# Kernel optimization log

Measured on AMD Instinct MI355X. Metric: run time of the kernel, lower is better.

Reference implementation:

```python
import jax, jax.numpy as jnp
import numpy as np

N_EMBD = 1024
N_HEAD = 16
HEAD_DIM = N_EMBD // N_HEAD


def setup_inputs() -> dict:
    key = jax.random.key(0)
    ks = jax.random.split(key, 9)
    B, T, C = 4, 2048, N_EMBD
    s = 1.0 / np.sqrt(C)
    return {
        "x": jax.random.normal(ks[0], (B, T, C), dtype=jnp.float32),
        "Wk": jax.random.normal(ks[1], (C, C), dtype=jnp.float32) * s,
        "bk": jax.random.normal(ks[2], (C,), dtype=jnp.float32) * 0.02,
        "Wq": jax.random.normal(ks[3], (C, C), dtype=jnp.float32) * s,
        "bq": jax.random.normal(ks[4], (C,), dtype=jnp.float32) * 0.02,
        "Wv": jax.random.normal(ks[5], (C, C), dtype=jnp.float32) * s,
        "bv": jax.random.normal(ks[6], (C,), dtype=jnp.float32) * 0.02,
        "Wp": jax.random.normal(ks[7], (C, C), dtype=jnp.float32) * s,
        "bp": jax.random.normal(ks[8], (C,), dtype=jnp.float32) * 0.02,
    }


def reference(x, Wk, bk, Wq, bq, Wv, bv, Wp, bp):
    B, T, C = x.shape
    nh, hs = N_HEAD, HEAD_DIM
    # linear projections; weights stored as [in, out] (x @ W + b)
    k = (x @ Wk + bk).reshape(B, T, nh, hs).transpose(0, 2, 1, 3)  # [B,nh,T,hs]
    q = (x @ Wq + bq).reshape(B, T, nh, hs).transpose(0, 2, 1, 3)
    v = (x @ Wv + bv).reshape(B, T, nh, hs).transpose(0, 2, 1, 3)
    att = jnp.einsum("bhqd,bhkd->bhqk", q, k) / jnp.sqrt(jnp.float32(hs))
    causal = jnp.tril(jnp.ones((T, T), dtype=bool))  # [T,T]
    att = jnp.where(causal[None, None], att, -jnp.inf)
    att = jax.nn.softmax(att, axis=-1)
    y = jnp.einsum("bhqk,bhkd->bhqd", att, v)  # [B,nh,T,hs]
    y = y.transpose(0, 2, 1, 3).reshape(B, T, C)
    return y @ Wp + bp
```

## Files before the change

### kernel.cpp

```cpp
#include <hip/hip_runtime.h>

#define TSEQ 2048
#define CDIM 1024
#define NH 16
#define HS 64
#define BATCH 4

typedef __attribute__((ext_vector_type(8))) short short8;
typedef __attribute__((ext_vector_type(4))) short s16x4;
typedef __attribute__((ext_vector_type(4))) float f32x4;

__device__ __forceinline__ short f2bf(float f) {
    unsigned u = __builtin_bit_cast(unsigned, f);
    unsigned r = (u + 0x7fffu + ((u >> 16) & 1u)) >> 16;
    return (short)r;
}

__device__ __forceinline__ void gload_lds16(const void* g, void* l) {
    __builtin_amdgcn_global_load_lds((const __attribute__((address_space(1))) void*)g,
                                     (__attribute__((address_space(3))) void*)l, 16, 0, 0);
}

__global__ void cvt_x(const float* __restrict__ x, short* __restrict__ o, int n4) {
    int i = blockIdx.x * 256 + threadIdx.x;
    if (i >= n4) return;
    float4 v = ((const float4*)x)[i];
    s16x4 r;
    r[0] = f2bf(v.x); r[1] = f2bf(v.y); r[2] = f2bf(v.z); r[3] = f2bf(v.w);
    ((s16x4*)o)[i] = r;
}

__global__ void wtrans(const float* __restrict__ Wk, const float* __restrict__ Wq,
                       const float* __restrict__ Wv, const float* __restrict__ Wp,
                       short* __restrict__ Wcat, short* __restrict__ Wpt) {
    const float* src; short* dst;
    if (blockIdx.z == 0)      { src = Wq; dst = Wcat; }
    else if (blockIdx.z == 1) { src = Wk; dst = Wcat + 1048576; }
    else if (blockIdx.z == 2) { src = Wv; dst = Wcat + 2097152; }
    else                      { src = Wp; dst = Wpt; }
    __shared__ float tl[64][65];
    int tx = threadIdx.x & 63, ty = threadIdx.x >> 6;
    int k0 = blockIdx.x * 64, n0 = blockIdx.y * 64;
#pragma unroll
    for (int i = 0; i < 16; ++i) {
        int r = i * 4 + ty;
        tl[r][tx] = src[(size_t)(k0 + r) * CDIM + n0 + tx];
    }
    __syncthreads();
#pragma unroll
    for (int i = 0; i < 16; ++i) {
        int r = i * 4 + ty;
        dst[(size_t)(n0 + r) * CDIM + k0 + tx] = f2bf(tl[tx][r]);
    }
}

__global__ void bias_pack(const float* __restrict__ bq, const float* __restrict__ bk,
                          const float* __restrict__ bv, float* __restrict__ bcat) {
    int i = blockIdx.x * 256 + threadIdx.x;
    if (i < 1024) bcat[i] = bq[i];
    else if (i < 2048) bcat[i] = bk[i - 1024];
    else if (i < 3072) bcat[i] = bv[i - 2048];
}

template <bool OUT_BF16>
__global__ __launch_bounds__(256) void gemm_bt(const short* __restrict__ A, int lda,
                                               const short* __restrict__ Bt,
                                               const float* __restrict__ bias,
                                               float alphaQ, int qcols,
                                               void* __restrict__ Cout, int ldc) {
    __shared__ short As[128 * 64];
    __shared__ short Bs[128 * 64];
    const int t = threadIdx.x;
    const int lane = t & 63, w = t >> 6;
    const int lr = lane & 15, lg = lane >> 4;
    const int wr = w >> 1, wc = w & 1;
    const int mbase = blockIdx.y * 128, nbase = blockIdx.x * 128;
    const float alpha = (nbase < qcols) ? alphaQ : 1.0f;
    f32x4 acc[4][4] = {};
    for (int k0 = 0; k0 < 1024; k0 += 64) {
#pragma unroll
        for (int i = 0; i < 4; ++i) {
            int chunk = i * 256 + t;
            int r = chunk >> 3, c = chunk & 7;
            int cl = c ^ (r & 7);
            gload_lds16(A + (size_t)(mbase + r) * lda + k0 + cl * 8, As + chunk * 8);
            gload_lds16(Bt + (size_t)(nbase + r) * 1024 + k0 + cl * 8, Bs + chunk * 8);
        }
        __syncthreads();
#pragma unroll
        for (int ks = 0; ks < 2; ++ks) {
            short8 a[4], b[4];
#pragma unroll
            for (int mi = 0; mi < 4; ++mi) {
                int row = wr * 64 + mi * 16 + lr;
                int ch = (ks * 4 + lg) ^ (row & 7);
                a[mi] = *(const short8*)(As + row * 64 + ch * 8);
            }
#pragma unroll
            for (int ni = 0; ni < 4; ++ni) {
                int row = wc * 64 + ni * 16 + lr;
                int ch = (ks * 4 + lg) ^ (row & 7);
                b[ni] = *(const short8*)(Bs + row * 64 + ch * 8);
            }
#pragma unroll
            for (int mi = 0; mi < 4; ++mi)
#pragma unroll
                for (int ni = 0; ni < 4; ++ni)
                    acc[mi][ni] = __builtin_amdgcn_mfma_f32_16x16x32_bf16(a[mi], b[ni],
                                                                          acc[mi][ni], 0, 0, 0);
        }
        __syncthreads();
    }
#pragma unroll
    for (int mi = 0; mi < 4; ++mi) {
#pragma unroll
        for (int ni = 0; ni < 4; ++ni) {
            int col = nbase + wc * 64 + ni * 16 + lr;
            float bv = bias[col];
#pragma unroll
            for (int i = 0; i < 4; ++i) {
                int row = mbase + wr * 64 + mi * 16 + lg * 4 + i;
                float v = (acc[mi][ni][i] + bv) * alpha;
                if (OUT_BF16)
                    ((short*)Cout)[(size_t)row * ldc + col] = f2bf(v);
                else
                    ((float*)Cout)[(size_t)row * ldc + col] = v;
            }
        }
    }
}

__global__ void vtrans(const short* __restrict__ QKV, short* __restrict__ Vt) {
    __shared__ short tl[64][68];
    const int t = threadIdx.x;
    const int tx = t & 63, ty = t >> 6;
    const int t0 = blockIdx.x * 64, bh = blockIdx.y;
    const int b = bh >> 4, h = bh & 15;
#pragma unroll
    for (int i = 0; i < 16; ++i) {
        int row = i * 4 + ty;
        tl[row][tx] = QKV[(size_t)(b * TSEQ + t0 + row) * 3072 + 2048 + h * HS + tx];
    }
    __syncthreads();
#pragma unroll
    for (int i = 0; i < 16; ++i) {
        int d = i * 4 + ty;
        Vt[(size_t)(bh * 64 + d) * TSEQ + t0 + tx] = tl[tx][d];
    }
}

__global__ __launch_bounds__(512, 4) void attn(const short* __restrict__ QKV,
                                               const short* __restrict__ Vt,
                                               short* __restrict__ Y) {
    __shared__ short Kl[2][64 * 64];
    __shared__ short Vl[2][64 * 64];
    __shared__ short Pl[8][16 * 64];
    const int t = threadIdx.x, lane = t & 63, w = t >> 6;
    const int lr = lane & 15, lg = lane >> 4;
    const int bh = blockIdx.x, b = bh >> 4, h = bh & 15;
    const int qt = 15 - blockIdx.y;
    const int q0w = qt * 128 + w * 16;
    const size_t rowbase = (size_t)b * TSEQ;
    const int niter = 2 * qt + 2;
    const float SHIFT2 = 17.31234049f;

    short8 qf[2];
#pragma unroll
    for (int ks = 0; ks < 2; ++ks)
        qf[ks] = *(const short8*)(QKV + (rowbase + q0w + lr) * 3072 + h * HS + ks * 32 + lg * 8);
    float l_i[4] = {0.f, 0.f, 0.f, 0.f};
    f32x4 o[4] = {};

    const int sr = t >> 3, sc = t & 7, scl = sc ^ (sr & 7);
    const short* Kg = QKV + 1024 + h * HS;
    gload_lds16(Kg + (rowbase + sr) * 3072 + scl * 8, &Kl[0][t * 8]);
    gload_lds16(Vt + (size_t)(bh * 64 + sr) * TSEQ + scl * 8, &Vl[0][t * 8]);
    __syncthreads();
    int buf = 0;
    for (int jt = 0; jt < niter; ++jt) {
        const int j0 = jt * 64;
        if (jt + 1 < niter) {
            const int j0n = j0 + 64;
            gload_lds16(Kg + (rowbase + j0n + sr) * 3072 + scl * 8, &Kl[buf ^ 1][t * 8]);
            gload_lds16(Vt + (size_t)(bh * 64 + sr) * TSEQ + j0n + scl * 8, &Vl[buf ^ 1][t * 8]);
        }
        if (j0 <= q0w + 15) {
            f32x4 s[4];
            __builtin_amdgcn_s_setprio(1);
#pragma unroll
            for (int nt = 0; nt < 4; ++nt) {
                s[nt] = f32x4{0.f, 0.f, 0.f, 0.f};
#pragma unroll
                for (int ks = 0; ks < 2; ++ks) {
                    short8 kf = *(const short8*)(&Kl[buf][(nt * 16 + lr) * 64 +
                                                          (((ks * 4 + lg) ^ (lr & 7)) * 8)]);
                    s[nt] = __builtin_amdgcn_mfma_f32_16x16x32_bf16(qf[ks], kf, s[nt], 0, 0, 0);
                }
            }
            __builtin_amdgcn_s_setprio(0);
            if (j0 + 63 > q0w) {
#pragma unroll
                for (int nt = 0; nt < 4; ++nt)
#pragma unroll
                    for (int i = 0; i < 4; ++i) {
                        int kv = j0 + nt * 16 + lr;
                        int q = q0w + lg * 4 + i;
                        if (kv > q) s[nt][i] = -__builtin_inff();
                    }
            }
#pragma unroll
            for (int i = 0; i < 4; ++i) {
                const int ql = lg * 4 + i;
                float pt[4];
#pragma unroll
                for (int nt = 0; nt < 4; ++nt) {
                    float p = __builtin_amdgcn_exp2f(s[nt][i] - SHIFT2);
                    unsigned u = __builtin_bit_cast(unsigned, p);
                    int chv = ((nt * 2 + (lr >> 3)) ^ (ql & 7));
                    Pl[w][ql * 64 + chv * 8 + (lr & 7)] = (short)(u >> 16);
                    pt[nt] = __builtin_bit_cast(float, u & 0xffff0000u);
                }
                l_i[i] += (pt[0] + pt[1]) + (pt[2] + pt[3]);
            }
            short8 pf[2];
#pragma unroll
            for (int ks = 0; ks < 2; ++ks)
                pf[ks] = *(const short8*)(&Pl[w][lr * 64 + (((ks * 4 + lg) ^ (lr & 7)) * 8)]);
            __builtin_amdgcn_s_setprio(1);
#pragma unroll
            for (int nd = 0; nd < 4; ++nd)
#pragma unroll
                for (int ks = 0; ks < 2; ++ks) {
                    short8 vf = *(const short8*)(&Vl[buf][(nd * 16 + lr) * 64 +
                                                          (((ks * 4 + lg) ^ (lr & 7)) * 8)]);
                    o[nd] = __builtin_amdgcn_mfma_f32_16x16x32_bf16(pf[ks], vf, o[nd], 0, 0, 0);
                }
            __builtin_amdgcn_s_setprio(0);
        }
        __syncthreads();
        buf ^= 1;
    }
#pragma unroll
    for (int i = 0; i < 4; ++i) {
        float l = l_i[i];
        l += __shfl_xor(l, 1);
        l += __shfl_xor(l, 2);
        l += __shfl_xor(l, 4);
        l += __shfl_xor(l, 8);
        float inv = 1.0f / l;
        int q = q0w + lg * 4 + i;
#pragma unroll
        for (int nd = 0; nd < 4; ++nd)
            Y[(rowbase + q) * 1024 + h * HS + nd * 16 + lr] = f2bf(o[nd][i] * inv);
    }
}

extern "C" void kernel_launch(void* const* d_in, const int* in_sizes, int n_in,
                              void* d_out, int out_size, void* d_ws, size_t ws_size,
                              hipStream_t stream) {
    const float* x  = (const float*)d_in[0];
    const float* Wk = (const float*)d_in[1];
    const float* bk = (const float*)d_in[2];
    const float* Wq = (const float*)d_in[3];
    const float* bq = (const float*)d_in[4];
    const float* Wv = (const float*)d_in[5];
    const float* bv = (const float*)d_in[6];
    const float* Wp = (const float*)d_in[7];
    const float* bp = (const float*)d_in[8];
    float* out = (float*)d_out;
    char* ws = (char*)d_ws;
    const size_t MB = 1024 * 1024;
    short* xb   = (short*)(ws);
    short* Wcat = (short*)(ws + 16 * MB);
    short* Wpt  = (short*)(ws + 22 * MB);
    short* QKVb = (short*)(ws + 24 * MB);
    short* Yb   = xb;
    short* VtT  = (short*)d_out;
    float* bcat = (float*)((char*)d_out + 16 * MB);

    const float alphaQ = 0.125f * 1.44269504088896f;

    cvt_x<<<8192, 256, 0, stream>>>(x, xb, 2097152);
    wtrans<<<dim3(16, 16, 4), 256, 0, stream>>>(Wk, Wq, Wv, Wp, Wcat, Wpt);
    bias_pack<<<12, 256, 0, stream>>>(bq, bk, bv, bcat);
    gemm_bt<true><<<dim3(24, 64), 256, 0, stream>>>(xb, 1024, Wcat, bcat, alphaQ, 1024,
                                                    QKVb, 3072);
    vtrans<<<dim3(32, 64), 256, 0, stream>>>(QKVb, VtT);
    attn<<<dim3(64, 16), 512, 0, stream>>>(QKVb, VtT, Yb);
    gemm_bt<false><<<dim3(8, 64), 256, 0, stream>>>(Yb, 1024, Wpt, bp, 1.0f, 0, out, 1024);
}
```

Baseline: 172.2 us.

## Replace GEMM with 256x256 double-buffered ping-pong pipelined kernel

Replaces the 128x128 single-buffered GEMM with a 256x256 tile, 8-wave kernel that double-buffers LDS and splits each k-step into four MFMA quadrants. Global-to-LDS loads for the next tiles are interleaved between quadrants, gated by explicit vmcnt waits and barriers, and MFMA sections run at raised priority. Block indices are swizzled to improve L2 locality. The aim is to raise data reuse and hide load latency, at the cost of fewer blocks (128 for the output projection, which may underfill the CUs) and fragile hand-counted waitcnt synchronisation.

```diff
diff --git a/kernel.cpp b/kernel.cpp
--- a/kernel.cpp
+++ b/kernel.cpp
@@ -20,6 +20,9 @@
     __builtin_amdgcn_global_load_lds((const __attribute__((address_space(1))) void*)g,
                                      (__attribute__((address_space(3))) void*)l, 16, 0, 0);
 }
+
+#define FENCE() asm volatile("" ::: "memory")
+#define BAR()  do { FENCE(); __builtin_amdgcn_s_barrier(); FENCE(); } while (0)
 
 __global__ void cvt_x(const float* __restrict__ x, short* __restrict__ o, int n4) {
     int i = blockIdx.x * 256 + threadIdx.x;
@@ -63,64 +66,141 @@
 }
 
 template <bool OUT_BF16>
-__global__ __launch_bounds__(256) void gemm_bt(const short* __restrict__ A, int lda,
-                                               const short* __restrict__ Bt,
-                                               const float* __restrict__ bias,
-                                               float alphaQ, int qcols,
-                                               void* __restrict__ Cout, int ldc) {
-    __shared__ short As[128 * 64];
-    __shared__ short Bs[128 * 64];
-    const int t = threadIdx.x;
-    const int lane = t & 63, w = t >> 6;
+__global__ __launch_bounds__(512, 2) void gemm256(const short* __restrict__ A,
+                                                  const short* __restrict__ Bt,
+                                                  const float* __restrict__ bias,
+                                                  float alphaQ, int qcols,
+                                                  void* __restrict__ Cout, int ldc,
+                                                  int ntN) {
+    __shared__ short As[2][16384];
+    __shared__ short Bs[2][16384];
+    const int t = threadIdx.x, lane = t & 63, w = t >> 6;
     const int lr = lane & 15, lg = lane >> 4;
-    const int wr = w >> 1, wc = w & 1;
-    const int mbase = blockIdx.y * 128, nbase = blockIdx.x * 128;
+    const int wr = w >> 2, wc = w & 3;
+    const int cpx = gridDim.x >> 3;
+    const int swz = (blockIdx.x & 7) * cpx + (blockIdx.x >> 3);
+    const int mbase = (swz / ntN) * 256, nbase = (swz % ntN) * 256;
     const float alpha = (nbase < qcols) ? alphaQ : 1.0f;
-    f32x4 acc[4][4] = {};
-    for (int k0 = 0; k0 < 1024; k0 += 64) {
-#pragma unroll
-        for (int i = 0; i < 4; ++i) {
-            int chunk = i * 256 + t;
-            int r = chunk >> 3, c = chunk & 7;
-            int cl = c ^ (r & 7);
-            gload_lds16(A + (size_t)(mbase + r) * lda + k0 + cl * 8, As + chunk * 8);
-            gload_lds16(Bt + (size_t)(nbase + r) * 1024 + k0 + cl * 8, Bs + chunk * 8);
-        }
-        __syncthreads();
-#pragma unroll
-        for (int ks = 0; ks < 2; ++ks) {
-            short8 a[4], b[4];
-#pragma unroll
-            for (int mi = 0; mi < 4; ++mi) {
-                int row = wr * 64 + mi * 16 + lr;
-                int ch = (ks * 4 + lg) ^ (row & 7);
-                a[mi] = *(const short8*)(As + row * 64 + ch * 8);
-            }
-#pragma unroll
-            for (int ni = 0; ni < 4; ++ni) {
-                int row = wc * 64 + ni * 16 + lr;
-                int ch = (ks * 4 + lg) ^ (row & 7);
-                b[ni] = *(const short8*)(Bs + row * 64 + ch * 8);
-            }
-#pragma unroll
-            for (int mi = 0; mi < 4; ++mi)
-#pragma unroll
-                for (int ni = 0; ni < 4; ++ni)
-                    acc[mi][ni] = __builtin_amdgcn_mfma_f32_16x16x32_bf16(a[mi], b[ni],
-                                                                          acc[mi][ni], 0, 0, 0);
-        }
-        __syncthreads();
-    }
-#pragma unroll
-    for (int mi = 0; mi < 4; ++mi) {
+    const int srow = t >> 3;
+    const int so8 = ((t & 7) ^ (srow & 7)) * 8;
+    const int c0 = (lg ^ (lr & 7)) * 8;
+    const int c1 = ((4 + lg) ^ (lr & 7)) * 8;
+    const int NT = 16;
+
+#define STAGE_A(buf, s, tc) gload_lds16(A + (size_t)(mbase + (s) * 64 + srow) * 1024 + (tc) * 64 + so8, \
+                                        &As[buf][(s) * 4096 + t * 8])
+#define STAGE_B(buf, s, tc) gload_lds16(Bt + (size_t)(nbase + (s) * 64 + srow) * 1024 + (tc) * 64 + so8, \
+                                        &Bs[buf][(s) * 4096 + t * 8])
+
+    f32x4 acc[8][4] = {};
+    short8 aL[2][4], aH[2][4], bA[2][2], bB[2][2];
+
+    STAGE_A(0, 0, 0); STAGE_A(0, 1, 0); STAGE_A(0, 2, 0); STAGE_A(0, 3, 0);
+    STAGE_B(0, 0, 0); STAGE_B(0, 1, 0); STAGE_B(0, 2, 0); STAGE_B(0, 3, 0);
+    STAGE_A(1, 0, 1); STAGE_A(1, 2, 1);
+    STAGE_B(1, 0, 1); STAGE_B(1, 1, 1); STAGE_B(1, 2, 1); STAGE_B(1, 3, 1);
+    asm volatile("s_waitcnt vmcnt(6)" ::: "memory");
+    __builtin_amdgcn_s_barrier();
+    FENCE();
+
+    for (int tau = 0; tau < NT; ++tau) {
+        const int p = tau & 1, q = p ^ 1;
+        const short* Ap = As[p];
+        const short* Bp = Bs[p];
+        const int t1 = (tau + 1 < NT) ? tau + 1 : NT - 1;
+        const int t2 = (tau + 2 < NT) ? tau + 2 : NT - 1;
+#pragma unroll
+        for (int mi = 0; mi < 4; ++mi) {
+            const int ao = (wr * 128 + mi * 16 + lr) * 64;
+            aL[0][mi] = *(const short8*)(Ap + ao + c0);
+            aL[1][mi] = *(const short8*)(Ap + ao + c1);
+        }
+#pragma unroll
+        for (int ni = 0; ni < 2; ++ni) {
+            const int bo = (wc * 64 + ni * 16 + lr) * 64;
+            bA[0][ni] = *(const short8*)(Bp + bo + c0);
+            bA[1][ni] = *(const short8*)(Bp + bo + c1);
+        }
+        STAGE_A(q, 1, t1); STAGE_A(q, 3, t1);
+        BAR();
+        __builtin_amdgcn_s_setprio(1);
+#pragma unroll
+        for (int mi = 0; mi < 4; ++mi)
+#pragma unroll
+            for (int ni = 0; ni < 2; ++ni)
+#pragma unroll
+                for (int ks = 0; ks < 2; ++ks)
+                    acc[mi][ni] = __builtin_amdgcn_mfma_f32_16x16x32_bf16(
+                        aL[ks][mi], bA[ks][ni], acc[mi][ni], 0, 0, 0);
+        __builtin_amdgcn_s_setprio(0);
+        BAR();
+#pragma unroll
+        for (int ni = 0; ni < 2; ++ni) {
+            const int bo = (wc * 64 + (ni + 2) * 16 + lr) * 64;
+            bB[0][ni] = *(const short8*)(Bp + bo + c0);
+            bB[1][ni] = *(const short8*)(Bp + bo + c1);
+        }
+        STAGE_A(p, 0, t2); STAGE_A(p, 2, t2);
+        BAR();
+        __builtin_amdgcn_s_setprio(1);
+#pragma unroll
+        for (int mi = 0; mi < 4; ++mi)
+#pragma unroll
+            for (int ni = 0; ni < 2; ++ni)
+#pragma unroll
+                for (int ks = 0; ks < 2; ++ks)
+                    acc[mi][ni + 2] = __builtin_amdgcn_mfma_f32_16x16x32_bf16(
+                        aL[ks][mi], bB[ks][ni], acc[mi][ni + 2], 0, 0, 0);
+        __builtin_amdgcn_s_setprio(0);
+        asm volatile("s_waitcnt vmcnt(10)" ::: "memory");
+        __builtin_amdgcn_s_barrier();
+        FENCE();
+#pragma unroll
+        for (int mi = 0; mi < 4; ++mi) {
+            const int ao = (wr * 128 + (mi + 4) * 16 + lr) * 64;
+            aH[0][mi] = *(const short8*)(Ap + ao + c0);
+            aH[1][mi] = *(const short8*)(Ap + ao + c1);
+        }
+        STAGE_B(p, 0, t2); STAGE_B(p, 1, t2);
+        BAR();
+        __builtin_amdgcn_s_setprio(1);
+#pragma unroll
+        for (int mi = 0; mi < 4; ++mi)
+#pragma unroll
+            for (int ni = 0; ni < 2; ++ni)
+#pragma unroll
+                for (int ks = 0; ks < 2; ++ks)
+                    acc[mi + 4][ni + 2] = __builtin_amdgcn_mfma_f32_16x16x32_bf16(
+                        aH[ks][mi], bB[ks][ni], acc[mi + 4][ni + 2], 0, 0, 0);
+        __builtin_amdgcn_s_setprio(0);
+        BAR();
+        STAGE_B(p, 2, t2); STAGE_B(p, 3, t2);
+        __builtin_amdgcn_s_setprio(1);
+#pragma unroll
+        for (int mi = 0; mi < 4; ++mi)
+#pragma unroll
+            for (int ni = 0; ni < 2; ++ni)
+#pragma unroll
+                for (int ks = 0; ks < 2; ++ks)
+                    acc[mi + 4][ni] = __builtin_amdgcn_mfma_f32_16x16x32_bf16(
+                        aH[ks][mi], bA[ks][ni], acc[mi + 4][ni], 0, 0, 0);
+        __builtin_amdgcn_s_setprio(0);
+        asm volatile("s_waitcnt vmcnt(8)" ::: "memory");
+        __builtin_amdgcn_s_barrier();
+        FENCE();
+    }
+#undef STAGE_A
+#undef STAGE_B
+#pragma unroll
+    for (int mi = 0; mi < 8; ++mi) {
 #pragma unroll
         for (int ni = 0; ni < 4; ++ni) {
-            int col = nbase + wc * 64 + ni * 16 + lr;
-            float bv = bias[col];
-#pragma unroll
-            for (int i = 0; i < 4; ++i) {
-                int row = mbase + wr * 64 + mi * 16 + lg * 4 + i;
-                float v = (acc[mi][ni][i] + bv) * alpha;
+            const int col = nbase + wc * 64 + ni * 16 + lr;
+            const float bv = bias[col];
+#pragma unroll
+            for (int ii = 0; ii < 4; ++ii) {
+                const int row = mbase + wr * 128 + mi * 16 + lg * 4 + ii;
+                const float v = (acc[mi][ni][ii] + bv) * alpha;
                 if (OUT_BF16)
                     ((short*)Cout)[(size_t)row * ldc + col] = f2bf(v);
                 else
@@ -283,9 +363,8 @@
     cvt_x<<<8192, 256, 0, stream>>>(x, xb, 2097152);
     wtrans<<<dim3(16, 16, 4), 256, 0, stream>>>(Wk, Wq, Wv, Wp, Wcat, Wpt);
     bias_pack<<<12, 256, 0, stream>>>(bq, bk, bv, bcat);
-    gemm_bt<true><<<dim3(24, 64), 256, 0, stream>>>(xb, 1024, Wcat, bcat, alphaQ, 1024,
-                                                    QKVb, 3072);
+    gemm256<true><<<384, 512, 0, stream>>>(xb, Wcat, bcat, alphaQ, 1024, QKVb, 3072, 12);
     vtrans<<<dim3(32, 64), 256, 0, stream>>>(QKVb, VtT);
     attn<<<dim3(64, 16), 512, 0, stream>>>(QKVb, VtT, Yb);
-    gemm_bt<false><<<dim3(8, 64), 256, 0, stream>>>(Yb, 1024, Wpt, bp, 1.0f, 0, out, 1024);
-}
+    gemm256<false><<<128, 512, 0, stream>>>(Yb, Wpt, bp, 1.0f, 0, out, 1024, 4);
+}
```

Result: slower. 190.4 us (+10.6%).

## Replace 128x128 GEMM with 256x256 double-buffered, phase-scheduled 8-wave GEMM

Applied to the files above, without the earlier changes.

Replaces the 128x128-tile, single-buffered GEMM with a 256x256-tile kernel using 512 threads and double-buffered LDS. Global-to-LDS loads for the next k-tiles are interleaved with four MFMA phases per tile, using explicit barriers, waitcnt gates and s_setprio so that memory traffic overlaps compute. Block indices are swizzled into groups for L2 locality. The larger tiles mean fewer blocks (384 and 128), which risks leaving CUs idle on the output projection, and correctness depends on the hand-tuned waitcnt counts.

```diff
diff --git a/kernel.cpp b/kernel.cpp
--- a/kernel.cpp
+++ b/kernel.cpp
@@ -20,6 +20,8 @@
     __builtin_amdgcn_global_load_lds((const __attribute__((address_space(1))) void*)g,
                                      (__attribute__((address_space(3))) void*)l, 16, 0, 0);
 }
+
+#define FENCE() asm volatile("" ::: "memory")
 
 __global__ void cvt_x(const float* __restrict__ x, short* __restrict__ o, int n4) {
     int i = blockIdx.x * 256 + threadIdx.x;
@@ -63,64 +65,146 @@
 }
 
 template <bool OUT_BF16>
-__global__ __launch_bounds__(256) void gemm_bt(const short* __restrict__ A, int lda,
-                                               const short* __restrict__ Bt,
-                                               const float* __restrict__ bias,
-                                               float alphaQ, int qcols,
-                                               void* __restrict__ Cout, int ldc) {
-    __shared__ short As[128 * 64];
-    __shared__ short Bs[128 * 64];
-    const int t = threadIdx.x;
-    const int lane = t & 63, w = t >> 6;
+__global__ __launch_bounds__(512, 2) void gemm256(const short* __restrict__ A,
+                                                  const short* __restrict__ Bt,
+                                                  const float* __restrict__ bias,
+                                                  float alphaQ, int qcols,
+                                                  void* __restrict__ Cout, int ldc,
+                                                  int ntN) {
+    __shared__ short As[2][16384];
+    __shared__ short Bs[2][16384];
+    const int t = threadIdx.x, lane = t & 63, w = t >> 6;
     const int lr = lane & 15, lg = lane >> 4;
-    const int wr = w >> 1, wc = w & 1;
-    const int mbase = blockIdx.y * 128, nbase = blockIdx.x * 128;
+    const int wr = w >> 2, wc = w & 3;
+    const int cpx = gridDim.x >> 3;
+    const int swz = (blockIdx.x & 7) * cpx + (blockIdx.x >> 3);
+    const int mbase = (swz / ntN) * 256, nbase = (swz % ntN) * 256;
     const float alpha = (nbase < qcols) ? alphaQ : 1.0f;
-    f32x4 acc[4][4] = {};
-    for (int k0 = 0; k0 < 1024; k0 += 64) {
-#pragma unroll
-        for (int i = 0; i < 4; ++i) {
-            int chunk = i * 256 + t;
-            int r = chunk >> 3, c = chunk & 7;
-            int cl = c ^ (r & 7);
-            gload_lds16(A + (size_t)(mbase + r) * lda + k0 + cl * 8, As + chunk * 8);
-            gload_lds16(Bt + (size_t)(nbase + r) * 1024 + k0 + cl * 8, Bs + chunk * 8);
-        }
-        __syncthreads();
-#pragma unroll
-        for (int ks = 0; ks < 2; ++ks) {
-            short8 a[4], b[4];
-#pragma unroll
-            for (int mi = 0; mi < 4; ++mi) {
-                int row = wr * 64 + mi * 16 + lr;
-                int ch = (ks * 4 + lg) ^ (row & 7);
-                a[mi] = *(const short8*)(As + row * 64 + ch * 8);
-            }
-#pragma unroll
-            for (int ni = 0; ni < 4; ++ni) {
-                int row = wc * 64 + ni * 16 + lr;
-                int ch = (ks * 4 + lg) ^ (row & 7);
-                b[ni] = *(const short8*)(Bs + row * 64 + ch * 8);
-            }
-#pragma unroll
-            for (int mi = 0; mi < 4; ++mi)
-#pragma unroll
-                for (int ni = 0; ni < 4; ++ni)
-                    acc[mi][ni] = __builtin_amdgcn_mfma_f32_16x16x32_bf16(a[mi], b[ni],
-                                                                          acc[mi][ni], 0, 0, 0);
-        }
-        __syncthreads();
-    }
-#pragma unroll
-    for (int mi = 0; mi < 4; ++mi) {
+    const int c0 = (lg ^ (lr & 7)) * 8;
+    const int c1 = ((4 + lg) ^ (lr & 7)) * 8;
+    const int sr = t >> 3, ss = t & 7;
+    const int sc0 = (ss ^ (sr & 7)) * 8;
+    const int NTILE = 16;
+
+#define STG_A(buf, h, kt) do { \
+    gload_lds16(A + (size_t)(mbase + (h) * 128 + sr) * 1024 + (kt) * 64 + sc0, \
+                &As[buf][(h) * 8192 + t * 8]); \
+    gload_lds16(A + (size_t)(mbase + (h) * 128 + 64 + sr) * 1024 + (kt) * 64 + sc0, \
+                &As[buf][(h) * 8192 + 4096 + t * 8]); \
+} while (0)
+#define STG_B(buf, h, kt) do { \
+    gload_lds16(Bt + (size_t)(nbase + (h) * 128 + sr) * 1024 + (kt) * 64 + sc0, \
+                &Bs[buf][(h) * 8192 + t * 8]); \
+    gload_lds16(Bt + (size_t)(nbase + (h) * 128 + 64 + sr) * 1024 + (kt) * 64 + sc0, \
+                &Bs[buf][(h) * 8192 + 4096 + t * 8]); \
+} while (0)
+#define DS_A(dst, p, mh) \
+    _Pragma("unroll") \
+    for (int mi = 0; mi < 4; ++mi) { \
+        const short* _b = &As[p][wr * 8192 + ((mh) * 64 + mi * 16 + lr) * 64]; \
+        dst[0][mi] = *(const short8*)(_b + c0); \
+        dst[1][mi] = *(const short8*)(_b + c1); \
+    }
+#define DS_B(dst, p, nh) \
+    _Pragma("unroll") \
+    for (int ni = 0; ni < 2; ++ni) { \
+        const short* _b = &Bs[p][(wc >> 1) * 8192 + \
+                                 ((wc & 1) * 64 + (nh) * 32 + ni * 16 + lr) * 64]; \
+        dst[0][ni] = *(const short8*)(_b + c0); \
+        dst[1][ni] = *(const short8*)(_b + c1); \
+    }
+#define MFMA16(mh, nh, af, bf) \
+    _Pragma("unroll") \
+    for (int mi = 0; mi < 4; ++mi) \
+        _Pragma("unroll") \
+        for (int ni = 0; ni < 2; ++ni) \
+            _Pragma("unroll") \
+            for (int ks = 0; ks < 2; ++ks) \
+                acc[(mh) * 4 + mi][(nh) * 2 + ni] = __builtin_amdgcn_mfma_f32_16x16x32_bf16( \
+                    af[ks][mi], bf[ks][ni], acc[(mh) * 4 + mi][(nh) * 2 + ni], 0, 0, 0);
+#define PH_MID() do { FENCE(); __builtin_amdgcn_s_barrier(); \
+    asm volatile("s_waitcnt lgkmcnt(0)" ::: "memory"); \
+    __builtin_amdgcn_sched_barrier(0); __builtin_amdgcn_s_setprio(1); } while (0)
+#define PH_END() do { __builtin_amdgcn_s_setprio(0); FENCE(); \
+    __builtin_amdgcn_s_barrier(); FENCE(); } while (0)
+#define PH_END_GATE() do { __builtin_amdgcn_s_setprio(0); \
+    asm volatile("s_waitcnt vmcnt(4)" ::: "memory"); \
+    __builtin_amdgcn_s_barrier(); FENCE(); } while (0)
+
+    f32x4 acc[8][4] = {};
+    short8 a0[2][4], a1[2][4], b0[2][2], b1[2][2];
+
+    STG_A(0, 0, 0); STG_A(0, 1, 0); STG_B(0, 0, 0); STG_B(0, 1, 0);
+    STG_A(1, 0, 1); STG_A(1, 1, 1);
+    asm volatile("s_waitcnt vmcnt(4)" ::: "memory");
+    __builtin_amdgcn_s_barrier();
+    FENCE();
+
+    for (int it = 0; it < 8; ++it) {
+        const int kt1 = 2 * it + 1;
+        const int kt2 = (2 * it + 2 < NTILE) ? 2 * it + 2 : NTILE - 1;
+        const int kt3 = (2 * it + 3 < NTILE) ? 2 * it + 3 : NTILE - 1;
+        DS_A(a0, 0, 0);
+        DS_B(b0, 0, 0);
+        STG_B(1, 0, kt1);
+        asm volatile("s_waitcnt lgkmcnt(8)" ::: "memory");
+        PH_MID();
+        MFMA16(0, 0, a0, b0);
+        PH_END();
+        DS_A(a1, 0, 1);
+        STG_B(1, 1, kt1);
+        PH_MID();
+        MFMA16(1, 0, a1, b0);
+        PH_END();
+        DS_B(b1, 0, 1);
+        STG_A(0, 0, kt2);
+        PH_MID();
+        MFMA16(1, 1, a1, b1);
+        PH_END();
+        STG_A(0, 1, kt2);
+        PH_MID();
+        MFMA16(0, 1, a0, b1);
+        PH_END_GATE();
+        DS_A(a0, 1, 0);
+        DS_B(b0, 1, 0);
+        STG_B(0, 0, kt2);
+        asm volatile("s_waitcnt lgkmcnt(8)" ::: "memory");
+        PH_MID();
+        MFMA16(0, 0, a0, b0);
+        PH_END();
+        DS_A(a1, 1, 1);
+        STG_B(0, 1, kt2);
+        PH_MID();
+        MFMA16(1, 0, a1, b0);
+        PH_END();
+        DS_B(b1, 1, 1);
+        STG_A(1, 0, kt3);
+        PH_MID();
+        MFMA16(1, 1, a1, b1);
+        PH_END();
+        STG_A(1, 1, kt3);
+        PH_MID();
+        MFMA16(0, 1, a0, b1);
+        PH_END_GATE();
+    }
+#undef STG_A
+#undef STG_B
+#undef DS_A
+#undef DS_B
+#undef MFMA16
+#undef PH_MID
+#undef PH_END
+#undef PH_END_GATE
+#pragma unroll
+    for (int mi = 0; mi < 8; ++mi) {
 #pragma unroll
         for (int ni = 0; ni < 4; ++ni) {
-            int col = nbase + wc * 64 + ni * 16 + lr;
-            float bv = bias[col];
-#pragma unroll
-            for (int i = 0; i < 4; ++i) {
-                int row = mbase + wr * 64 + mi * 16 + lg * 4 + i;
-                float v = (acc[mi][ni][i] + bv) * alpha;
+            const int col = nbase + wc * 64 + ni * 16 + lr;
+            const float bv = bias[col];
+#pragma unroll
+            for (int ii = 0; ii < 4; ++ii) {
+                const int row = mbase + wr * 128 + mi * 16 + lg * 4 + ii;
+                const float v = (acc[mi][ni][ii] + bv) * alpha;
                 if (OUT_BF16)
                     ((short*)Cout)[(size_t)row * ldc + col] = f2bf(v);
                 else
@@ -283,9 +367,8 @@
     cvt_x<<<8192, 256, 0, stream>>>(x, xb, 2097152);
     wtrans<<<dim3(16, 16, 4), 256, 0, stream>>>(Wk, Wq, Wv, Wp, Wcat, Wpt);
     bias_pack<<<12, 256, 0, stream>>>(bq, bk, bv, bcat);
-    gemm_bt<true><<<dim3(24, 64), 256, 0, stream>>>(xb, 1024, Wcat, bcat, alphaQ, 1024,
-                                                    QKVb, 3072);
+    gemm256<true><<<384, 512, 0, stream>>>(xb, Wcat, bcat, alphaQ, 1024, QKVb, 3072, 12);
     vtrans<<<dim3(32, 64), 256, 0, stream>>>(QKVb, VtT);
     attn<<<dim3(64, 16), 512, 0, stream>>>(QKVb, VtT, Yb);
-    gemm_bt<false><<<dim3(8, 64), 256, 0, stream>>>(Yb, 1024, Wpt, bp, 1.0f, 0, out, 1024);
-}
+    gemm256<false><<<128, 512, 0, stream>>>(Yb, Wpt, bp, 1.0f, 0, out, 1024, 4);
+}
```

Result: slower. 198.0 us (+15.0%).
